# Optimization experiments

Measured on AMD Instinct MI355X. Metric: run time of the kernel, lower is better.

## Reference

```python
import jax, jax.numpy as jnp
import numpy as np


def _binop(ei, ej):
    # diagonal linear recurrence combine: (a_i, b_i) * (a_j, b_j) -> (a_j*a_i, a_j*b_i + b_j)
    ai, bi = ei
    aj, bj = ej
    return aj * ai, aj * bi + bj


def setup_inputs() -> dict:
    key = jax.random.key(0)
    ks = jax.random.split(key, 9)
    B_, T, D_in, D_out, N = 16, 2048, 512, 512, 512
    inp = {
        "input": jax.random.normal(ks[0], (B_, T, D_in), dtype=jnp.float32),
        "D": jax.random.normal(ks[1], (D_out, D_in), dtype=jnp.float32) / np.sqrt(D_in),
        "nu_log": jax.random.normal(ks[2], (N,), dtype=jnp.float32),
        "theta_log": jax.random.normal(ks[3], (N,), dtype=jnp.float32),
        "gamma_log": jax.random.normal(ks[4], (N,), dtype=jnp.float32),
        "B_re": jax.random.normal(ks[5], (N, D_in), dtype=jnp.float32) / np.sqrt(2 * D_in),
        "B_im": jax.random.normal(ks[6], (N, D_in), dtype=jnp.float32) / np.sqrt(2 * D_in),
        "C_re": jax.random.normal(ks[7], (D_out, N), dtype=jnp.float32) / np.sqrt(N),
        "C_im": jax.random.normal(ks[8], (D_out, N), dtype=jnp.float32) / np.sqrt(N),
    }
    return inp


def reference(input, D, nu_log, theta_log, gamma_log, B_re, B_im, C_re, C_im):
    # ss_params
    lam_abs = jnp.exp(-jnp.exp(nu_log))                      # [N]
    lam_phase = jnp.exp(theta_log)                           # [N]
    lam = lam_abs * (jnp.cos(lam_phase) + 1j * jnp.sin(lam_phase))  # complex [N]
    gamma = jnp.exp(gamma_log)                               # [N]
    Bc = (B_re + 1j * B_im) * gamma[:, None]                 # [N, D_in]
    Cc = C_re + 1j * C_im                                    # [D_out, N]

    # input projection: Bu_elements [batch, T, N] (complex)
    Bu = input.astype(Bc.dtype) @ Bc.T
    lam_el = jnp.broadcast_to(lam, Bu.shape)

    # parallel associative scan over time axis (initial state is zero)
    _, states = jax.lax.associative_scan(_binop, (lam_el, Bu), axis=1)

    # readout
    y = jnp.real(states @ Cc.T) + input @ D.T                # [batch, T, D_out]
    return y
```

## Files before the change

### kernel.cpp

```cpp
#include <hip/hip_runtime.h>
#include <hip/hip_fp16.h>

typedef _Float16 f16;
typedef __attribute__((ext_vector_type(8))) _Float16 f16x8;
typedef __attribute__((ext_vector_type(2))) _Float16 f16x2;
typedef __attribute__((ext_vector_type(4))) float f32x4;

#define B_SZ 16
#define T_SZ 2048
#define DIN 512
#define DOUT 512
#define N_SZ 512
#define M_SZ (B_SZ * T_SZ)
#define LCHUNK 64
#define NCHUNK 32

__device__ __forceinline__ void gload_lds16(const void* g, void* l) {
  __builtin_amdgcn_global_load_lds(
      (const __attribute__((address_space(1))) void*)g,
      (__attribute__((address_space(3))) void*)l, 16, 0, 0);
}


__global__ void prep_all(const float* __restrict__ nu_log,
                         const float* __restrict__ theta_log,
                         const float* __restrict__ gamma_log,
                         const float* __restrict__ B_re, const float* __restrict__ B_im,
                         const float* __restrict__ C_re, const float* __restrict__ C_im,
                         const float* __restrict__ Dm, const float* __restrict__ input,
                         float2* __restrict__ lam2, float2* __restrict__ lamL2,
                         float2* __restrict__ lamp,
                         f16* __restrict__ W1, f16* __restrict__ W2,
                         f16* __restrict__ inp16) {
  int b = blockIdx.x;
  if (b < 2) {
    int n = b * 256 + threadIdx.x;
    float nu = expf(nu_log[n]);
    float ph = expf(theta_log[n]);
    float la = expf(-nu);
    lam2[n] = make_float2(la * cosf(ph), la * sinf(ph));
    float laL = expf(-nu * (float)LCHUNK);
    float phL = ph * (float)LCHUNK;
    lamL2[n] = make_float2(laL * cosf(phL), laL * sinf(phL));
  } else if (b < 4) {
    int n = (b - 2) * 256 + threadIdx.x;
    float nu = expf(nu_log[n]);
    float ph = expf(theta_log[n]);
    float la = expf(-nu);
    float2 l1 = make_float2(la * cosf(ph), la * sinf(ph));
    float2 cur = l1;
    for (int j = 0; j < LCHUNK; ++j) {
      lamp[(size_t)j * 512 + n] = cur;
      float nre = cur.x * l1.x - cur.y * l1.y;
      cur.y = cur.x * l1.y + cur.y * l1.x;
      cur.x = nre;
    }
  } else if (b < 4 + 2048) {
    int tid = (b - 4) * 256 + threadIdx.x;
    int np = tid >> 9;
    int d = tid & 511;
    int n = np >> 1;
    float g = expf(gamma_log[n]);
    const float* src = (np & 1) ? B_im : B_re;
    W1[(size_t)np * 512 + d] = (f16)(src[(size_t)n * 512 + d] * g);
  } else if (b < 4 + 2048 + 3072) {
    int tid = (b - 2052) * 256 + threadIdx.x;
    int j = tid / 1536;
    int k = tid - j * 1536;
    float v;
    if (k < 1024) {
      int n = k >> 1;
      v = (k & 1) ? -C_im[(size_t)j * 512 + n] : C_re[(size_t)j * 512 + n];
    } else {
      v = Dm[(size_t)j * 512 + (k - 1024)];
    }
    W2[(size_t)j * 1536 + k] = (f16)v;
  } else {
    int tid = (b - 5124) * 256 + threadIdx.x;
    int m = tid >> 6;
    int d0 = (tid & 63) << 3;
    const float4* p = (const float4*)(input + (size_t)m * DIN + d0);
    float4 a = p[0], c = p[1];
    f16x8 h;
    h[0] = (f16)a.x; h[1] = (f16)a.y; h[2] = (f16)a.z; h[3] = (f16)a.w;
    h[4] = (f16)c.x; h[5] = (f16)c.y; h[6] = (f16)c.z; h[7] = (f16)c.w;
    *(f16x8*)(inp16 + (size_t)m * 512 + d0) = h;
  }
}


__global__ void scan_b(const float2* __restrict__ S, const float2* __restrict__ lamL2,
                       float2* __restrict__ Carry) {
  int tid = blockIdx.x * 256 + threadIdx.x;
  int n = tid & 511;
  int b = tid >> 9;
  float2 lL = lamL2[n];
  float cre = 0.f, cim = 0.f;
  for (int c = 0; c < NCHUNK; ++c) {
    size_t idx = (size_t)(b * NCHUNK + c) * 512 + n;
    Carry[idx] = make_float2(cre, cim);
    float2 s = S[idx];
    float nre = lL.x * cre - lL.y * cim + s.x;
    cim = lL.x * cim + lL.y * cre + s.y;
    cre = nre;
  }
}


template <typename CT, bool FUSE, bool CARRY>
__global__ __launch_bounds__(512, 2) void gemm256(
    const f16* __restrict__ A, int lda,
    const f16* __restrict__ Bm, int ldb,
    CT* __restrict__ C, int ldc, int K, int nxt,
    const float2* __restrict__ lam2, unsigned* __restrict__ sloc_out,
    float2* __restrict__ Svec,
    const unsigned* __restrict__ sloc_in, const float2* __restrict__ lamp,
    const float2* __restrict__ Carry) {
  extern __shared__ f16 smem[];
  f16* sA = smem;
  f16* sB = smem + 2 * 16384;

  const int tid = threadIdx.x;
  const int lane = tid & 63;
  const int wid = tid >> 6;
  const int wr = wid >> 2;
  const int wc = wid & 3;
  const int fr = lane & 15;
  const int fg = lane >> 4;
  const int xr = fr & 7;

  const int nwg = gridDim.x;
  const int id = blockIdx.x;
  const int swz = (id & 7) * (nwg >> 3) + (id >> 3);
  const int m0 = (swz / nxt) * 256;
  const int n0 = (swz % nxt) * 256;

  const int srow = tid >> 3;
  const int scol = ((tid & 7) ^ (srow & 7)) * 8;
  const int sdst = wid * 512;

  const int NT = K >> 6;

  f32x4 acc[8][4];
#pragma unroll
  for (int i = 0; i < 8; ++i)
#pragma unroll
    for (int j = 0; j < 4; ++j) acc[i][j] = f32x4{0.f, 0.f, 0.f, 0.f};

  const int ar0 = wr * 128;
  const int bc0 = wc * 64;

  auto stageB = [&](int t) {
    f16* dB = sB + (t & 1) * 16384 + sdst;
    const f16* gB = Bm + (size_t)(n0 + srow) * ldb + t * 64 + scol;
    gload_lds16(gB, dB);
    gload_lds16(gB + (size_t)64 * ldb, dB + 4096);
    gload_lds16(gB + (size_t)128 * ldb, dB + 8192);
    gload_lds16(gB + (size_t)192 * ldb, dB + 12288);
  };
  auto stageA_g = [&](int t) {
    f16* dA = sA + (t & 1) * 16384 + sdst;
    const int kc = CARRY ? (t - 16) * 64 : t * 64;
    const f16* gA = A + (size_t)(m0 + srow) * lda + kc + scol;
    gload_lds16(gA, dA);
    gload_lds16(gA + (size_t)64 * lda, dA + 4096);
    gload_lds16(gA + (size_t)128 * lda, dA + 8192);
    gload_lds16(gA + (size_t)192 * lda, dA + 12288);
  };

  uint4 sl[4];
  float2 lpq[4];
  float2 crq[4][4];

  auto cstage_issue = [&](int t) {
    const int nq0 = t * 32 + (scol >> 1);
    const unsigned* sp = sloc_in + (size_t)(m0 + srow) * 512 + nq0;
    const float2* lpp = lamp + (size_t)srow * 512 + nq0;
    const float2* crp = Carry + (size_t)(m0 >> 6) * 512 + nq0;
#pragma unroll
    for (int q = 0; q < 4; ++q) lpq[q] = lpp[q];
#pragma unroll
    for (int i = 0; i < 4; ++i) {
      sl[i] = *(const uint4*)(sp + (size_t)i * 64 * 512);
#pragma unroll
      for (int q = 0; q < 4; ++q) crq[i][q] = crp[(size_t)i * 512 + q];
    }
  };
  auto cstage_finish = [&](int t) {
    f16* dst = sA + (t & 1) * 16384 + tid * 8;
#pragma unroll
    for (int i = 0; i < 4; ++i) {
      unsigned u4[4] = {sl[i].x, sl[i].y, sl[i].z, sl[i].w};
      f16x8 o;
#pragma unroll
      for (int q = 0; q < 4; ++q) {
        f16x2 u = __builtin_bit_cast(f16x2, u4[q]);
        float lx = lpq[q].x, ly = lpq[q].y;
        float cx = crq[i][q].x, cy = crq[i][q].y;
        o[2 * q] = (f16)((float)u.x + lx * cx - ly * cy);
        o[2 * q + 1] = (f16)((float)u.y + lx * cy + ly * cx);
      }
      *(f16x8*)(dst + i * 4096) = o;
    }
  };

  auto stage_issue = [&](int t) {
    stageB(t);
    if (CARRY && t < 16)
      cstage_issue(t);
    else
      stageA_g(t);
  };

  auto barrier = [&]() {
    __builtin_amdgcn_sched_barrier(0);
    __builtin_amdgcn_s_barrier();
    __builtin_amdgcn_sched_barrier(0);
  };

  stage_issue(0);
  if (CARRY) {
    cstage_finish(0);
    asm volatile("s_waitcnt vmcnt(0) lgkmcnt(0)" ::: "memory");
  } else {
    asm volatile("s_waitcnt vmcnt(0)" ::: "memory");
  }
  barrier();

  f16x8 bf[4][2];
  for (int t = 0; t < NT; ++t) {
    const int b = t & 1;
    const f16* bA = sA + b * 16384;
    const f16* bB = sB + b * 16384;
    if (t + 1 < NT) stage_issue(t + 1);
#pragma unroll
    for (int h = 0; h < 4; ++h) {
      if (h == 0) {
#pragma unroll
        for (int nrep = 0; nrep < 4; ++nrep)
#pragma unroll
          for (int ks = 0; ks < 2; ++ks) {
            int row = bc0 + nrep * 16 + fr;
            bf[nrep][ks] =
                *(const f16x8*)(bB + row * 64 + (((ks * 4 + fg) ^ xr) * 8));
          }
      }
      f16x8 af[2][2];
#pragma unroll
      for (int mi = 0; mi < 2; ++mi)
#pragma unroll
        for (int ks = 0; ks < 2; ++ks) {
          int row = ar0 + (h * 2 + mi) * 16 + fr;
          af[mi][ks] =
              *(const f16x8*)(bA + row * 64 + (((ks * 4 + fg) ^ xr) * 8));
        }
      __builtin_amdgcn_s_setprio(1);
#pragma unroll
      for (int mi = 0; mi < 2; ++mi)
#pragma unroll
        for (int nrep = 0; nrep < 4; ++nrep)
#pragma unroll
          for (int ks = 0; ks < 2; ++ks)
            acc[h * 2 + mi][nrep] = __builtin_amdgcn_mfma_f32_16x16x32_f16(
                af[mi][ks], bf[nrep][ks], acc[h * 2 + mi][nrep], 0, 0, 0);
      __builtin_amdgcn_s_setprio(0);
      if (h == 3 && t + 1 < NT) {
        if (CARRY && t + 1 < 16) {
          cstage_finish(t + 1);
          asm volatile("s_waitcnt vmcnt(0) lgkmcnt(0)" ::: "memory");
        } else {
          asm volatile("s_waitcnt vmcnt(0)" ::: "memory");
        }
      }
      barrier();
    }
  }

  if constexpr (FUSE) {
    f16* reg = smem + wid * 8192;
#pragma unroll
    for (int mi = 0; mi < 8; ++mi)
#pragma unroll
      for (int ni = 0; ni < 4; ++ni)
#pragma unroll
        for (int r = 0; r < 4; ++r)
          reg[(mi * 16 + fg * 4 + r) * 64 + ni * 16 + fr] = (f16)acc[mi][ni][r];
    __syncthreads();
    const int half = lane >> 5;
    const int nc = lane & 31;
    const int n = ((n0 + wc * 64) >> 1) + nc;
    const float2 l2 = lam2[n];
    const f16* col = smem + wid * 8192 + (half * 64) * 64 + 2 * nc;
    const int mbase = m0 + wr * 128 + half * 64;
    unsigned* sp = sloc_out + (size_t)mbase * 512 + n;
    float sre = 0.f, sim = 0.f;
#pragma unroll 1
    for (int j0 = 0; j0 < 64; j0 += 8) {
      f16x2 u[8];
#pragma unroll
      for (int q = 0; q < 8; ++q) u[q] = *(const f16x2*)(col + (j0 + q) * 64);
#pragma unroll
      for (int q = 0; q < 8; ++q) {
        float nre = l2.x * sre - l2.y * sim + (float)u[q].x;
        sim = l2.x * sim + l2.y * sre + (float)u[q].y;
        sre = nre;
        f16x2 o;
        o.x = (f16)sre;
        o.y = (f16)sim;
        sp[(size_t)(j0 + q) * 512] = __builtin_bit_cast(unsigned, o);
      }
    }
    Svec[(size_t)((m0 >> 11) * NCHUNK + ((mbase >> 6) & (NCHUNK - 1))) * 512 + n] =
        make_float2(sre, sim);
  } else {
#pragma unroll
    for (int mi = 0; mi < 8; ++mi) {
      int rbase = m0 + ar0 + mi * 16 + fg * 4;
#pragma unroll
      for (int ni = 0; ni < 4; ++ni) {
        int col = n0 + bc0 + ni * 16 + fr;
#pragma unroll
        for (int r = 0; r < 4; ++r)
          C[(size_t)(rbase + r) * ldc + col] = (CT)acc[mi][ni][r];
      }
    }
  }
}


extern "C" void kernel_launch(void* const* d_in, const int* in_sizes, int n_in,
                              void* d_out, int out_size, void* d_ws, size_t ws_size,
                              hipStream_t stream) {
  const float* input = (const float*)d_in[0];
  const float* Dmat = (const float*)d_in[1];
  const float* nu_log = (const float*)d_in[2];
  const float* theta_log = (const float*)d_in[3];
  const float* gamma_log = (const float*)d_in[4];
  const float* B_re = (const float*)d_in[5];
  const float* B_im = (const float*)d_in[6];
  const float* C_re = (const float*)d_in[7];
  const float* C_im = (const float*)d_in[8];
  float* y = (float*)d_out;

  char* ws = (char*)d_ws;
  size_t off = 0;
  auto alloc = [&](size_t bytes) {
    void* p = ws + off;
    off = (off + bytes + 255) & ~(size_t)255;
    return p;
  };
  float2* lam2 = (float2*)alloc(N_SZ * sizeof(float2));
  float2* lamL2 = (float2*)alloc(N_SZ * sizeof(float2));
  float2* lamp = (float2*)alloc((size_t)LCHUNK * N_SZ * sizeof(float2));
  f16* W1 = (f16*)alloc((size_t)2 * N_SZ * DIN * 2);
  f16* W2 = (f16*)alloc((size_t)DOUT * 1536 * 2);
  f16* inp16 = (f16*)alloc((size_t)M_SZ * DIN * 2);
  unsigned* sloc = (unsigned*)alloc((size_t)M_SZ * N_SZ * 4);
  float2* S = (float2*)alloc((size_t)B_SZ * NCHUNK * N_SZ * sizeof(float2));
  float2* Carry = (float2*)alloc((size_t)B_SZ * NCHUNK * N_SZ * sizeof(float2));

  const int shmem = 131072;
  {
    auto* g1 = gemm256<f16, true, false>;
    auto* g2 = gemm256<float, false, true>;
    hipFuncSetAttribute((const void*)g1,
                        hipFuncAttributeMaxDynamicSharedMemorySize, shmem);
    hipFuncSetAttribute((const void*)g2,
                        hipFuncAttributeMaxDynamicSharedMemorySize, shmem);
  }

  prep_all<<<13316, 256, 0, stream>>>(nu_log, theta_log, gamma_log, B_re, B_im,
                                      C_re, C_im, Dmat, input, lam2, lamL2, lamp,
                                      W1, W2, inp16);

  gemm256<f16, true, false><<<512, 512, shmem, stream>>>(
      inp16, 512, W1, 512, (f16*)nullptr, 0, 512, 4, lam2, sloc, S,
      nullptr, nullptr, nullptr);

  scan_b<<<(B_SZ * N_SZ) / 256, 256, 0, stream>>>(S, lamL2, Carry);

  gemm256<float, false, true><<<256, 512, shmem, stream>>>(
      inp16, 512, W2, 1536, y, 512, 1536, 2, nullptr, nullptr, nullptr,
      sloc, lamp, Carry);
}
```

Measured before the change: 141.8 us.

## Split readout GEMM into dedicated 128x128-tile kernel with more workgroups

The templated 256x256 GEMM is split into two specialised kernels. The first-stage fused GEMM keeps its 256-tile design with constants hard-coded. The readout GEMM now uses 128x128 tiles, 256 threads and 64 KB of LDS, launching 1024 workgroups instead of 256. This gives more parallelism and better CU occupancy on the readout, at the cost of lower per-tile data reuse and more redundant carry/lamp loads per output.

```diff
diff --git a/kernel.cpp b/kernel.cpp
--- a/kernel.cpp
+++ b/kernel.cpp
@@ -107,18 +107,14 @@
 }
 
 
-template <typename CT, bool FUSE, bool CARRY>
-__global__ __launch_bounds__(512, 2) void gemm256(
-    const f16* __restrict__ A, int lda,
-    const f16* __restrict__ Bm, int ldb,
-    CT* __restrict__ C, int ldc, int K, int nxt,
+__global__ __launch_bounds__(512, 2) void gemm_fuse(
+    const f16* __restrict__ A, const f16* __restrict__ Bm,
     const float2* __restrict__ lam2, unsigned* __restrict__ sloc_out,
-    float2* __restrict__ Svec,
-    const unsigned* __restrict__ sloc_in, const float2* __restrict__ lamp,
-    const float2* __restrict__ Carry) {
+    float2* __restrict__ Svec) {
   extern __shared__ f16 smem[];
   f16* sA = smem;
   f16* sB = smem + 2 * 16384;
+  const int lda = 512, ldb = 512, K = 512, nxt = 4;
 
   const int tid = threadIdx.x;
   const int lane = tid & 63;
@@ -138,7 +134,6 @@
   const int srow = tid >> 3;
   const int scol = ((tid & 7) ^ (srow & 7)) * 8;
   const int sdst = wid * 512;
-
   const int NT = K >> 6;
 
   f32x4 acc[8][4];
@@ -150,67 +145,21 @@
   const int ar0 = wr * 128;
   const int bc0 = wc * 64;
 
-  auto stageB = [&](int t) {
-    f16* dB = sB + (t & 1) * 16384 + sdst;
+  auto stage = [&](int t) {
+    const int b = t & 1;
+    f16* dA = sA + b * 16384 + sdst;
+    f16* dB = sB + b * 16384 + sdst;
+    const f16* gA = A + (size_t)(m0 + srow) * lda + t * 64 + scol;
     const f16* gB = Bm + (size_t)(n0 + srow) * ldb + t * 64 + scol;
+    gload_lds16(gA, dA);
+    gload_lds16(gA + (size_t)64 * lda, dA + 4096);
+    gload_lds16(gA + (size_t)128 * lda, dA + 8192);
+    gload_lds16(gA + (size_t)192 * lda, dA + 12288);
     gload_lds16(gB, dB);
     gload_lds16(gB + (size_t)64 * ldb, dB + 4096);
     gload_lds16(gB + (size_t)128 * ldb, dB + 8192);
     gload_lds16(gB + (size_t)192 * ldb, dB + 12288);
   };
-  auto stageA_g = [&](int t) {
-    f16* dA = sA + (t & 1) * 16384 + sdst;
-    const int kc = CARRY ? (t - 16) * 64 : t * 64;
-    const f16* gA = A + (size_t)(m0 + srow) * lda + kc + scol;
-    gload_lds16(gA, dA);
-    gload_lds16(gA + (size_t)64 * lda, dA + 4096);
-    gload_lds16(gA + (size_t)128 * lda, dA + 8192);
-    gload_lds16(gA + (size_t)192 * lda, dA + 12288);
-  };
-
-  uint4 sl[4];
-  float2 lpq[4];
-  float2 crq[4][4];
-
-  auto cstage_issue = [&](int t) {
-    const int nq0 = t * 32 + (scol >> 1);
-    const unsigned* sp = sloc_in + (size_t)(m0 + srow) * 512 + nq0;
-    const float2* lpp = lamp + (size_t)srow * 512 + nq0;
-    const float2* crp = Carry + (size_t)(m0 >> 6) * 512 + nq0;
-#pragma unroll
-    for (int q = 0; q < 4; ++q) lpq[q] = lpp[q];
-#pragma unroll
-    for (int i = 0; i < 4; ++i) {
-      sl[i] = *(const uint4*)(sp + (size_t)i * 64 * 512);
-#pragma unroll
-      for (int q = 0; q < 4; ++q) crq[i][q] = crp[(size_t)i * 512 + q];
-    }
-  };
-  auto cstage_finish = [&](int t) {
-    f16* dst = sA + (t & 1) * 16384 + tid * 8;
-#pragma unroll
-    for (int i = 0; i < 4; ++i) {
-      unsigned u4[4] = {sl[i].x, sl[i].y, sl[i].z, sl[i].w};
-      f16x8 o;
-#pragma unroll
-      for (int q = 0; q < 4; ++q) {
-        f16x2 u = __builtin_bit_cast(f16x2, u4[q]);
-        float lx = lpq[q].x, ly = lpq[q].y;
-        float cx = crq[i][q].x, cy = crq[i][q].y;
-        o[2 * q] = (f16)((float)u.x + lx * cx - ly * cy);
-        o[2 * q + 1] = (f16)((float)u.y + lx * cy + ly * cx);
-      }
-      *(f16x8*)(dst + i * 4096) = o;
-    }
-  };
-
-  auto stage_issue = [&](int t) {
-    stageB(t);
-    if (CARRY && t < 16)
-      cstage_issue(t);
-    else
-      stageA_g(t);
-  };
 
   auto barrier = [&]() {
     __builtin_amdgcn_sched_barrier(0);
@@ -218,13 +167,8 @@
     __builtin_amdgcn_sched_barrier(0);
   };
 
-  stage_issue(0);
-  if (CARRY) {
-    cstage_finish(0);
-    asm volatile("s_waitcnt vmcnt(0) lgkmcnt(0)" ::: "memory");
-  } else {
-    asm volatile("s_waitcnt vmcnt(0)" ::: "memory");
-  }
+  stage(0);
+  asm volatile("s_waitcnt vmcnt(0)" ::: "memory");
   barrier();
 
   f16x8 bf[4][2];
@@ -232,7 +176,7 @@
     const int b = t & 1;
     const f16* bA = sA + b * 16384;
     const f16* bB = sB + b * 16384;
-    if (t + 1 < NT) stage_issue(t + 1);
+    if (t + 1 < NT) stage(t + 1);
 #pragma unroll
     for (int h = 0; h < 4; ++h) {
       if (h == 0) {
@@ -264,65 +208,197 @@
             acc[h * 2 + mi][nrep] = __builtin_amdgcn_mfma_f32_16x16x32_f16(
                 af[mi][ks], bf[nrep][ks], acc[h * 2 + mi][nrep], 0, 0, 0);
       __builtin_amdgcn_s_setprio(0);
-      if (h == 3 && t + 1 < NT) {
-        if (CARRY && t + 1 < 16) {
-          cstage_finish(t + 1);
-          asm volatile("s_waitcnt vmcnt(0) lgkmcnt(0)" ::: "memory");
-        } else {
-          asm volatile("s_waitcnt vmcnt(0)" ::: "memory");
-        }
+      if (h == 3 && t + 1 < NT)
+        asm volatile("s_waitcnt vmcnt(0)" ::: "memory");
+      barrier();
+    }
+  }
+
+  f16* reg = smem + wid * 8192;
+#pragma unroll
+  for (int mi = 0; mi < 8; ++mi)
+#pragma unroll
+    for (int ni = 0; ni < 4; ++ni)
+#pragma unroll
+      for (int r = 0; r < 4; ++r)
+        reg[(mi * 16 + fg * 4 + r) * 64 + ni * 16 + fr] = (f16)acc[mi][ni][r];
+  __syncthreads();
+  const int half = lane >> 5;
+  const int nc = lane & 31;
+  const int n = ((n0 + wc * 64) >> 1) + nc;
+  const float2 l2 = lam2[n];
+  const f16* col = smem + wid * 8192 + (half * 64) * 64 + 2 * nc;
+  const int mbase = m0 + wr * 128 + half * 64;
+  unsigned* sp = sloc_out + (size_t)mbase * 512 + n;
+  float sre = 0.f, sim = 0.f;
+#pragma unroll 1
+  for (int j0 = 0; j0 < 64; j0 += 8) {
+    f16x2 u[8];
+#pragma unroll
+    for (int q = 0; q < 8; ++q) u[q] = *(const f16x2*)(col + (j0 + q) * 64);
+#pragma unroll
+    for (int q = 0; q < 8; ++q) {
+      float nre = l2.x * sre - l2.y * sim + (float)u[q].x;
+      sim = l2.x * sim + l2.y * sre + (float)u[q].y;
+      sre = nre;
+      f16x2 o;
+      o.x = (f16)sre;
+      o.y = (f16)sim;
+      sp[(size_t)(j0 + q) * 512] = __builtin_bit_cast(unsigned, o);
+    }
+  }
+  Svec[(size_t)((m0 >> 11) * NCHUNK + ((mbase >> 6) & (NCHUNK - 1))) * 512 + n] =
+      make_float2(sre, sim);
+}
+
+
+__global__ __launch_bounds__(256, 2) void gemm_ro(
+    const f16* __restrict__ inp16, const f16* __restrict__ W2,
+    float* __restrict__ C,
+    const unsigned* __restrict__ sloc, const float2* __restrict__ lamp,
+    const float2* __restrict__ Carry) {
+  extern __shared__ f16 smem[];
+  const int ldb = 1536, ldc = 512, NT = 24;
+
+  const int tid = threadIdx.x;
+  const int lane = tid & 63;
+  const int wid = tid >> 6;
+  const int wr = wid >> 1;
+  const int wc = wid & 1;
+  const int fr = lane & 15;
+  const int fg = lane >> 4;
+  const int xr = fr & 7;
+
+  const int nwg = gridDim.x;
+  const int id = blockIdx.x;
+  const int swz = (id & 7) * (nwg >> 3) + (id >> 3);
+  const int m0 = (swz >> 2) * 128;
+  const int n0 = (swz & 3) * 128;
+
+  const int srow = tid >> 3;
+  const int slot = (tid & 7) ^ (srow & 7);
+  const int scol = slot * 8;
+  const int sdst = wid * 512;
+
+  f32x4 acc[4][4];
+#pragma unroll
+  for (int i = 0; i < 4; ++i)
+#pragma unroll
+    for (int j = 0; j < 4; ++j) acc[i][j] = f32x4{0.f, 0.f, 0.f, 0.f};
+
+  auto stageB = [&](int t) {
+    f16* dB = smem + (t & 1) * 16384 + 8192 + sdst;
+    const f16* gB = W2 + (size_t)(n0 + srow) * ldb + t * 64 + scol;
+#pragma unroll
+    for (int i = 0; i < 4; ++i)
+      gload_lds16(gB + (size_t)(32 * i) * ldb, dB + i * 2048);
+  };
+  auto stageA_g = [&](int t) {
+    f16* dA = smem + (t & 1) * 16384 + sdst;
+    const f16* gA = inp16 + (size_t)(m0 + srow) * 512 + (t - 16) * 64 + scol;
+#pragma unroll
+    for (int i = 0; i < 4; ++i)
+      gload_lds16(gA + (size_t)(32 * i) * 512, dA + i * 2048);
+  };
+
+  uint4 sl[4];
+  float2 lpq[2][4];
+  float2 crq[2][4];
+
+  auto cstage_issue = [&](int t) {
+    const int nq = t * 32 + slot * 4;
+    const unsigned* sp = sloc + (size_t)(m0 + srow) * 512 + nq;
+#pragma unroll
+    for (int i = 0; i < 4; ++i)
+      sl[i] = *(const uint4*)(sp + (size_t)(32 * i) * 512);
+#pragma unroll
+    for (int p = 0; p < 2; ++p) {
+      const float2* lpp = lamp + (size_t)(srow + 32 * p) * 512 + nq;
+      const float2* crp = Carry + (size_t)((m0 >> 6) + p) * 512 + nq;
+#pragma unroll
+      for (int q = 0; q < 4; ++q) {
+        lpq[p][q] = lpp[q];
+        crq[p][q] = crp[q];
       }
-      barrier();
-    }
-  }
-
-  if constexpr (FUSE) {
-    f16* reg = smem + wid * 8192;
-#pragma unroll
-    for (int mi = 0; mi < 8; ++mi)
+    }
+  };
+  auto cstage_finish = [&](int t) {
+    f16* dA = smem + (t & 1) * 16384;
+#pragma unroll
+    for (int i = 0; i < 4; ++i) {
+      unsigned u4[4] = {sl[i].x, sl[i].y, sl[i].z, sl[i].w};
+      f16x8 o;
+#pragma unroll
+      for (int q = 0; q < 4; ++q) {
+        f16x2 u = __builtin_bit_cast(f16x2, u4[q]);
+        float lx = lpq[i & 1][q].x, ly = lpq[i & 1][q].y;
+        float cx = crq[i >> 1][q].x, cy = crq[i >> 1][q].y;
+        o[2 * q] = (f16)((float)u.x + lx * cx - ly * cy);
+        o[2 * q + 1] = (f16)((float)u.y + lx * cy + ly * cx);
+      }
+      *(f16x8*)(dA + (srow + 32 * i) * 64 + (tid & 7) * 8) = o;
+    }
+  };
+
+  auto stage_issue = [&](int t) {
+    stageB(t);
+    if (t < 16)
+      cstage_issue(t);
+    else
+      stageA_g(t);
+  };
+
+  stage_issue(0);
+  cstage_finish(0);
+  asm volatile("s_waitcnt vmcnt(0) lgkmcnt(0)" ::: "memory");
+  __builtin_amdgcn_sched_barrier(0);
+  __builtin_amdgcn_s_barrier();
+  __builtin_amdgcn_sched_barrier(0);
+
+  for (int t = 0; t < NT; ++t) {
+    const f16* bA = smem + (t & 1) * 16384;
+    const f16* bB = bA + 8192;
+    if (t + 1 < NT) stage_issue(t + 1);
+
+    f16x8 af[4][2], bf[4][2];
+#pragma unroll
+    for (int mi = 0; mi < 4; ++mi)
+#pragma unroll
+      for (int ks = 0; ks < 2; ++ks)
+        af[mi][ks] = *(const f16x8*)(bA + (wr * 64 + mi * 16 + fr) * 64 +
+                                     (((ks * 4 + fg) ^ xr) * 8));
+#pragma unroll
+    for (int ni = 0; ni < 4; ++ni)
+#pragma unroll
+      for (int ks = 0; ks < 2; ++ks)
+        bf[ni][ks] = *(const f16x8*)(bB + (wc * 64 + ni * 16 + fr) * 64 +
+                                     (((ks * 4 + fg) ^ xr) * 8));
+    __builtin_amdgcn_s_setprio(1);
+#pragma unroll
+    for (int mi = 0; mi < 4; ++mi)
 #pragma unroll
       for (int ni = 0; ni < 4; ++ni)
 #pragma unroll
-        for (int r = 0; r < 4; ++r)
-          reg[(mi * 16 + fg * 4 + r) * 64 + ni * 16 + fr] = (f16)acc[mi][ni][r];
-    __syncthreads();
-    const int half = lane >> 5;
-    const int nc = lane & 31;
-    const int n = ((n0 + wc * 64) >> 1) + nc;
-    const float2 l2 = lam2[n];
-    const f16* col = smem + wid * 8192 + (half * 64) * 64 + 2 * nc;
-    const int mbase = m0 + wr * 128 + half * 64;
-    unsigned* sp = sloc_out + (size_t)mbase * 512 + n;
-    float sre = 0.f, sim = 0.f;
-#pragma unroll 1
-    for (int j0 = 0; j0 < 64; j0 += 8) {
-      f16x2 u[8];
-#pragma unroll
-      for (int q = 0; q < 8; ++q) u[q] = *(const f16x2*)(col + (j0 + q) * 64);
-#pragma unroll
-      for (int q = 0; q < 8; ++q) {
-        float nre = l2.x * sre - l2.y * sim + (float)u[q].x;
-        sim = l2.x * sim + l2.y * sre + (float)u[q].y;
-        sre = nre;
-        f16x2 o;
-        o.x = (f16)sre;
-        o.y = (f16)sim;
-        sp[(size_t)(j0 + q) * 512] = __builtin_bit_cast(unsigned, o);
-      }
-    }
-    Svec[(size_t)((m0 >> 11) * NCHUNK + ((mbase >> 6) & (NCHUNK - 1))) * 512 + n] =
-        make_float2(sre, sim);
-  } else {
-#pragma unroll
-    for (int mi = 0; mi < 8; ++mi) {
-      int rbase = m0 + ar0 + mi * 16 + fg * 4;
-#pragma unroll
-      for (int ni = 0; ni < 4; ++ni) {
-        int col = n0 + bc0 + ni * 16 + fr;
-#pragma unroll
-        for (int r = 0; r < 4; ++r)
-          C[(size_t)(rbase + r) * ldc + col] = (CT)acc[mi][ni][r];
-      }
+        for (int ks = 0; ks < 2; ++ks)
+          acc[mi][ni] = __builtin_amdgcn_mfma_f32_16x16x32_f16(
+              af[mi][ks], bf[ni][ks], acc[mi][ni], 0, 0, 0);
+    __builtin_amdgcn_s_setprio(0);
+    if (t + 1 < NT && t + 1 < 16) cstage_finish(t + 1);
+    asm volatile("s_waitcnt vmcnt(0) lgkmcnt(0)" ::: "memory");
+    __builtin_amdgcn_sched_barrier(0);
+    __builtin_amdgcn_s_barrier();
+    __builtin_amdgcn_sched_barrier(0);
+  }
+
+#pragma unroll
+  for (int mi = 0; mi < 4; ++mi) {
+    int rbase = m0 + wr * 64 + mi * 16 + fg * 4;
+#pragma unroll
+    for (int ni = 0; ni < 4; ++ni) {
+      int col = n0 + wc * 64 + ni * 16 + fr;
+#pragma unroll
+      for (int r = 0; r < 4; ++r)
+        C[(size_t)(rbase + r) * ldc + col] = acc[mi][ni][r];
     }
   }
 }
@@ -359,27 +435,20 @@
   float2* S = (float2*)alloc((size_t)B_SZ * NCHUNK * N_SZ * sizeof(float2));
   float2* Carry = (float2*)alloc((size_t)B_SZ * NCHUNK * N_SZ * sizeof(float2));
 
-  const int shmem = 131072;
   {
-    auto* g1 = gemm256<f16, true, false>;
-    auto* g2 = gemm256<float, false, true>;
-    hipFuncSetAttribute((const void*)g1,
-                        hipFuncAttributeMaxDynamicSharedMemorySize, shmem);
-    hipFuncSetAttribute((const void*)g2,
-                        hipFuncAttributeMaxDynamicSharedMemorySize, shmem);
+    hipFuncSetAttribute((const void*)gemm_fuse,
+                        hipFuncAttributeMaxDynamicSharedMemorySize, 131072);
+    hipFuncSetAttribute((const void*)gemm_ro,
+                        hipFuncAttributeMaxDynamicSharedMemorySize, 65536);
   }
 
   prep_all<<<13316, 256, 0, stream>>>(nu_log, theta_log, gamma_log, B_re, B_im,
                                       C_re, C_im, Dmat, input, lam2, lamL2, lamp,
                                       W1, W2, inp16);
 
-  gemm256<f16, true, false><<<512, 512, shmem, stream>>>(
-      inp16, 512, W1, 512, (f16*)nullptr, 0, 512, 4, lam2, sloc, S,
-      nullptr, nullptr, nullptr);
+  gemm_fuse<<<512, 512, 131072, stream>>>(inp16, W1, lam2, sloc, S);
 
   scan_b<<<(B_SZ * N_SZ) / 256, 256, 0, stream>>>(S, lamL2, Carry);
 
-  gemm256<float, false, true><<<256, 512, shmem, stream>>>(
-      inp16, 512, W2, 1536, y, 512, 1536, 2, nullptr, nullptr, nullptr,
-      sloc, lamp, Carry);
-}
+  gemm_ro<<<1024, 256, 65536, stream>>>(inp16, W2, y, sloc, lamp, Carry);
+}
```

Result: slower. 150.4 us (+6.0%).
